# Kernel optimization log

Measured on AMD Instinct MI355X. Metric: run time of the kernel, lower is better.

Reference implementation:

```python
import jax, jax.numpy as jnp
import numpy as np
import math

B, SEQ_IN, D_IN = 4, 1028, 64
D = 1024          # hidden_size
H = 16            # num_heads
HD = D // H       # head_dim
L = 4             # num_layers
D_OUT = 1
EPS = 1e-6


def setup_inputs() -> dict:
    key = jax.random.key(0)
    ks = iter(jax.random.split(key, 32))
    s = 0.02
    inp = {}
    inp['x'] = jax.random.normal(next(ks), (B, SEQ_IN, D_IN), jnp.float32)
    # conv frontend (torch Conv1d weight layout: [out_ch, in_ch, k])
    inp['conv1_w'] = jax.random.normal(next(ks), (D // 2, D_IN, 3), jnp.float32) * s
    inp['conv1_b'] = jnp.zeros((D // 2,), jnp.float32)
    inp['conv2_w'] = jax.random.normal(next(ks), (D, D // 2, 3), jnp.float32) * s
    inp['conv2_b'] = jnp.zeros((D,), jnp.float32)
    # stacked per-layer params [L, ...]
    inp['lnA_w'] = jnp.ones((L, D), jnp.float32)
    inp['lnA_b'] = jnp.zeros((L, D), jnp.float32)
    inp['q_w'] = jax.random.normal(next(ks), (L, D, D), jnp.float32) * s
    inp['q_b'] = jnp.zeros((L, D), jnp.float32)
    inp['k_w'] = jax.random.normal(next(ks), (L, D, D), jnp.float32) * s
    inp['k_b'] = jnp.zeros((L, D), jnp.float32)
    inp['v_w'] = jax.random.normal(next(ks), (L, D, D), jnp.float32) * s
    inp['v_b'] = jnp.zeros((L, D), jnp.float32)
    inp['o_w'] = jax.random.normal(next(ks), (L, D, D), jnp.float32) * s
    inp['o_b'] = jnp.zeros((L, D), jnp.float32)
    inp['lnB_w'] = jnp.ones((L, D), jnp.float32)
    inp['lnB_b'] = jnp.zeros((L, D), jnp.float32)
    inp['f1_w'] = jax.random.normal(next(ks), (L, 2 * D, D), jnp.float32) * s
    inp['f1_b'] = jnp.zeros((L, 2 * D), jnp.float32)
    inp['f2_w'] = jax.random.normal(next(ks), (L, D, 2 * D), jnp.float32) * s
    inp['f2_b'] = jnp.zeros((L, D), jnp.float32)
    inp['fc_w'] = jax.random.normal(next(ks), (D_OUT, D), jnp.float32) * s
    inp['fc_b'] = jnp.zeros((D_OUT,), jnp.float32)
    return inp


def _layernorm(x, w, b):
    # torch-style: unbiased std (ddof=1), eps added to std (not var)
    mean = jnp.mean(x, axis=-1, keepdims=True)
    var = jnp.sum((x - mean) ** 2, axis=-1, keepdims=True) / (x.shape[-1] - 1)
    return w * ((x - mean) / (jnp.sqrt(var) + EPS)) + b


def _pos_encoding(S, d):
    pos = jnp.arange(S, dtype=jnp.float32)[:, None]
    div = jnp.exp(jnp.arange(0, d, 2, dtype=jnp.float32) * (-math.log(10000.0) / d))
    pe = jnp.zeros((S, d), jnp.float32)
    pe = pe.at[:, 0::2].set(jnp.sin(pos * div))
    pe = pe.at[:, 1::2].set(jnp.cos(pos * div))
    return pe


def _forward(x, conv1_w, conv1_b, conv2_w, conv2_b,
             lnA_w, lnA_b, q_w, q_b, k_w, k_b, v_w, v_b, o_w, o_b,
             lnB_w, lnB_b, f1_w, f1_b, f2_w, f2_b, fc_w, fc_b):
    dn = ('NCH', 'OIH', 'NCH')
    h = jnp.transpose(x, (0, 2, 1))                       # [B, D_in, S_in]
    h = jax.lax.conv_general_dilated(h, conv1_w, (1,), 'VALID', dimension_numbers=dn) + conv1_b[None, :, None]
    h = jax.lax.conv_general_dilated(h, conv2_w, (1,), 'VALID', dimension_numbers=dn) + conv2_b[None, :, None]
    h = jnp.transpose(h, (0, 2, 1))                       # [B, S, D]
    S = h.shape[1]
    h = h + _pos_encoding(S, D)[None]
    scale = 1.0 / math.sqrt(HD)

    def layer(xc, p):
        (lnaw, lnab, qw, qb, kw, kb, vw, vb, ow, ob,
         lnbw, lnbb, f1w, f1b, f2w, f2b) = p
        hn = _layernorm(xc, lnaw, lnab)
        q = (hn @ qw.T + qb).reshape(B, S, H, HD).transpose(0, 2, 1, 3)
        k = (hn @ kw.T + kb).reshape(B, S, H, HD).transpose(0, 2, 1, 3)
        v = (hn @ vw.T + vb).reshape(B, S, H, HD).transpose(0, 2, 1, 3)
        scores = jnp.einsum('bhsd,bhtd->bhst', q, k) * scale
        attn = scores / (1.0 + jnp.abs(scores))           # softsign, NOT softmax
        wv = jnp.einsum('bhst,bhtd->bhsd', attn, v)
        wv = wv.transpose(0, 2, 1, 3).reshape(B, S, D)
        xc = xc + (wv @ ow.T + ob)
        hn2 = _layernorm(xc, lnbw, lnbb)
        ff = jax.nn.relu(hn2 @ f1w.T + f1b) @ f2w.T + f2b
        return xc + ff, None

    params = (lnA_w, lnA_b, q_w, q_b, k_w, k_b, v_w, v_b, o_w, o_b,
              lnB_w, lnB_b, f1_w, f1_b, f2_w, f2_b)
    h, _ = jax.lax.scan(layer, h, params)
    pooled = jnp.mean(h, axis=1)                          # [B, D]
    return pooled @ fc_w.T + fc_b                         # [B, D_OUT]


def reference(x, conv1_w, conv1_b, conv2_w, conv2_b,
              lnA_w, lnA_b, q_w, q_b, k_w, k_b, v_w, v_b, o_w, o_b,
              lnB_w, lnB_b, f1_w, f1_b, f2_w, f2_b, fc_w, fc_b):
    return _forward(x, conv1_w, conv1_b, conv2_w, conv2_b,
                    lnA_w, lnA_b, q_w, q_b, k_w, k_b, v_w, v_b, o_w, o_b,
                    lnB_w, lnB_b, f1_w, f1_b, f2_w, f2_b, fc_w, fc_b)
```

## Files before the change

### kernel.cpp

```cpp
#include <hip/hip_runtime.h>
#include <hip/hip_bf16.h>
#include <math.h>

typedef __bf16 v8bf __attribute__((ext_vector_type(8)));
typedef float  v4f  __attribute__((ext_vector_type(4)));
typedef unsigned short v8us __attribute__((ext_vector_type(8)));

__device__ __forceinline__ unsigned short f2bfu(float f) {
    unsigned u = __builtin_bit_cast(unsigned, f);
    unsigned r = (u + 0x7fffu + ((u >> 16) & 1u)) >> 16;
    return (unsigned short)r;
}
__device__ __forceinline__ float bf2f(unsigned short u) {
    unsigned x = ((unsigned)u) << 16;
    return __builtin_bit_cast(float, x);
}

__device__ __forceinline__ long long swidx(int r, int k, int kt ) {
    return ((long long)((r >> 4) * kt + (k >> 5)) << 9)
         + (((k >> 3) & 3) << 7) + ((r & 15) << 3) + (k & 7);
}

#define GLDS16(g, s)                                                        \
    __builtin_amdgcn_global_load_lds(                                       \
        (const __attribute__((address_space(1))) void*)(g),                 \
        (__attribute__((address_space(3))) void*)(s), 16, 0, 0)

__global__ __launch_bounds__(256) void gemm_sw_k(
    const unsigned short* __restrict__ Asw,
    const unsigned short* __restrict__ Bsw,
    const float* __restrict__ bias,
    const float* __restrict__ res,
    float* __restrict__ Cf,
    unsigned short* __restrict__ Cb,
    unsigned short* __restrict__ Csw,
    unsigned short* __restrict__ Ct, int ctcol0,
    int M, int N, int K, int ldC, int relu)
{
    __shared__ __align__(16) unsigned short As[2][8][512];
    __shared__ __align__(16) unsigned short Bs[2][8][512];
    const int t = threadIdx.x;
    const int w = t >> 6;
    const int l = t & 63;

    int bx = blockIdx.x, by = blockIdx.y;
    {
        int nbx = gridDim.x;
        int nb  = nbx * gridDim.y;
        if ((nb & 7) == 0) {
            int bid = by * nbx + bx;
            int nid = (bid & 7) * (nb >> 3) + (bid >> 3);
            by = nid / nbx;
            bx = nid - by * nbx;
        }
    }
    const int m0 = by * 128;
    const int n0 = bx * 128;
    const int r16 = l & 15;
    const int qb  = l >> 4;
    const int wm = w >> 1, wn = w & 1;
    const int kt = K >> 5;

    const unsigned short* gA0 = Asw + (((long long)((m0 >> 4) + 2 * w) * kt) << 9) + l * 8;
    const unsigned short* gA1 = gA0 + ((long long)kt << 9);
    const unsigned short* gB0 = Bsw + (((long long)((n0 >> 4) + 2 * w) * kt) << 9) + l * 8;
    const unsigned short* gB1 = gB0 + ((long long)kt << 9);

    v4f acc[4][4];
#pragma unroll
    for (int i = 0; i < 4; i++)
#pragma unroll
        for (int j = 0; j < 4; j++) acc[i][j] = (v4f){0.f, 0.f, 0.f, 0.f};

    GLDS16(gA0, &As[0][2 * w + 0][0]);
    GLDS16(gA1, &As[0][2 * w + 1][0]);
    GLDS16(gB0, &Bs[0][2 * w + 0][0]);
    GLDS16(gB1, &Bs[0][2 * w + 1][0]);
    __syncthreads();

    int cur = 0;
    for (int c = 1; c < kt; c++) {
        const long long o = (long long)c << 9;
        GLDS16(gA0 + o, &As[cur ^ 1][2 * w + 0][0]);
        GLDS16(gA1 + o, &As[cur ^ 1][2 * w + 1][0]);
        GLDS16(gB0 + o, &Bs[cur ^ 1][2 * w + 0][0]);
        GLDS16(gB1 + o, &Bs[cur ^ 1][2 * w + 1][0]);
        v8bf af[4], bfr[4];
#pragma unroll
        for (int i = 0; i < 4; i++) af[i]  = *(const v8bf*)(&As[cur][4 * wm + i][l * 8]);
#pragma unroll
        for (int j = 0; j < 4; j++) bfr[j] = *(const v8bf*)(&Bs[cur][4 * wn + j][l * 8]);
#pragma unroll
        for (int i = 0; i < 4; i++)
#pragma unroll
            for (int j = 0; j < 4; j++)
                acc[i][j] = __builtin_amdgcn_mfma_f32_16x16x32_bf16(
                    af[i], bfr[j], acc[i][j], 0, 0, 0);
        __syncthreads();
        cur ^= 1;
    }
    {
        v8bf af[4], bfr[4];
#pragma unroll
        for (int i = 0; i < 4; i++) af[i]  = *(const v8bf*)(&As[cur][4 * wm + i][l * 8]);
#pragma unroll
        for (int j = 0; j < 4; j++) bfr[j] = *(const v8bf*)(&Bs[cur][4 * wn + j][l * 8]);
#pragma unroll
        for (int i = 0; i < 4; i++)
#pragma unroll
            for (int j = 0; j < 4; j++)
                acc[i][j] = __builtin_amdgcn_mfma_f32_16x16x32_bf16(
                    af[i], bfr[j], acc[i][j], 0, 0, 0);
    }

    float bv[4];
#pragma unroll
    for (int j = 0; j < 4; j++) bv[j] = bias[n0 + 64 * wn + 16 * j + r16];
    const int colbase = n0 + 64 * wn + r16;
    const int nt = N >> 5;
#pragma unroll
    for (int i = 0; i < 4; i++) {
        int rowb = m0 + 64 * wm + 16 * i + qb * 4;
#pragma unroll
        for (int j = 0; j < 4; j++) {
            int col = colbase + 16 * j;
            float v[4];
#pragma unroll
            for (int r = 0; r < 4; r++) v[r] = acc[i][j][r] + bv[j];
            if (Ct && col >= ctcol0) {
                ushort4 o;
                o.x = f2bfu(v[0]); o.y = f2bfu(v[1]);
                o.z = f2bfu(v[2]); o.w = f2bfu(v[3]);
                *(ushort4*)(Ct + ((long long)(rowb >> 10) << 20)
                            + (long long)(col - ctcol0) * 1024 + (rowb & 1023)) = o;
            } else if (Csw) {
#pragma unroll
                for (int r = 0; r < 4; r++) {
                    int row = rowb + r;
                    float vv = v[r];
                    if (relu) vv = fmaxf(vv, 0.f);
                    Csw[swidx(row, col, nt)] = f2bfu(vv);
                }
            } else {
#pragma unroll
                for (int r = 0; r < 4; r++) {
                    int row = rowb + r;
                    long long off = (long long)row * ldC + col;
                    float vv = v[r];
                    if (res)  vv += res[off];
                    if (relu) vv = fmaxf(vv, 0.f);
                    if (Cf) Cf[off] = vv;
                    if (Cb) ((unsigned short*)Cb)[off] = f2bfu(vv);
                }
            }
        }
    }
}

__global__ __launch_bounds__(256) void gemm_mfma_k(
    const __hip_bfloat16* __restrict__ A, int rpbA, long long bstrideA, int ldA,
    const __hip_bfloat16* __restrict__ B,
    const float* __restrict__ bias,
    const float* __restrict__ res,
    float* __restrict__ Cf,
    __hip_bfloat16* __restrict__ Cb,
    int M, int N, int K, int ldC, int relu)
{
    __shared__ __align__(16) __hip_bfloat16 As[2][8][64][8];
    __shared__ __align__(16) __hip_bfloat16 Bs[2][4][64][8];
    const int t  = threadIdx.x;
    const int w  = t >> 6;
    const int l  = t & 63;
    const int m0 = blockIdx.y * 128;
    const int n0 = blockIdx.x * 64;
    const int r16 = l & 15;
    const int qb  = l >> 4;
    const int wm = w >> 1, wn = w & 1;

    const __hip_bfloat16* gA[2];
#pragma unroll
    for (int tt = 0; tt < 2; tt++) {
        int arow = m0 + 16 * (2 * w + tt) + r16;
        gA[tt] = A + (long long)(arow / rpbA) * bstrideA
                   + (long long)(arow % rpbA) * ldA + qb * 8;
    }
    const __hip_bfloat16* gB = B + (long long)(n0 + 16 * w + r16) * K + qb * 8;

    v4f acc[4][2];
#pragma unroll
    for (int i = 0; i < 4; i++)
#pragma unroll
        for (int j = 0; j < 2; j++) acc[i][j] = (v4f){0.f, 0.f, 0.f, 0.f};

    GLDS16(gA[0], &As[0][2 * w + 0][0][0]);
    GLDS16(gA[1], &As[0][2 * w + 1][0][0]);
    GLDS16(gB,    &Bs[0][w][0][0]);
    __syncthreads();

    int cur = 0;
    for (int k0 = 32; k0 < K; k0 += 32) {
        v8bf af[4], bfr[2];
#pragma unroll
        for (int i = 0; i < 4; i++) af[i]  = *(const v8bf*)(&As[cur][4 * wm + i][l][0]);
#pragma unroll
        for (int j = 0; j < 2; j++) bfr[j] = *(const v8bf*)(&Bs[cur][2 * wn + j][l][0]);
        GLDS16(gA[0] + k0, &As[cur ^ 1][2 * w + 0][0][0]);
        GLDS16(gA[1] + k0, &As[cur ^ 1][2 * w + 1][0][0]);
        GLDS16(gB + k0,    &Bs[cur ^ 1][w][0][0]);
#pragma unroll
        for (int i = 0; i < 4; i++)
#pragma unroll
            for (int j = 0; j < 2; j++)
                acc[i][j] = __builtin_amdgcn_mfma_f32_16x16x32_bf16(
                    af[i], bfr[j], acc[i][j], 0, 0, 0);
        __syncthreads();
        cur ^= 1;
    }
    {
        v8bf af[4], bfr[2];
#pragma unroll
        for (int i = 0; i < 4; i++) af[i]  = *(const v8bf*)(&As[cur][4 * wm + i][l][0]);
#pragma unroll
        for (int j = 0; j < 2; j++) bfr[j] = *(const v8bf*)(&Bs[cur][2 * wn + j][l][0]);
#pragma unroll
        for (int i = 0; i < 4; i++)
#pragma unroll
            for (int j = 0; j < 2; j++)
                acc[i][j] = __builtin_amdgcn_mfma_f32_16x16x32_bf16(
                    af[i], bfr[j], acc[i][j], 0, 0, 0);
    }

    float bv[2];
#pragma unroll
    for (int j = 0; j < 2; j++) bv[j] = bias[n0 + 32 * wn + 16 * j + r16];
    const int colbase = n0 + 32 * wn + r16;
#pragma unroll
    for (int i = 0; i < 4; i++) {
        int rowb = m0 + 64 * wm + 16 * i + qb * 4;
#pragma unroll
        for (int j = 0; j < 2; j++) {
            int col = colbase + 16 * j;
#pragma unroll
            for (int r = 0; r < 4; r++) {
                int row = rowb + r;
                if (row >= M) continue;
                long long off = (long long)row * ldC + col;
                float vv = acc[i][j][r] + bv[j];
                if (res)  vv += res[off];
                if (relu) vv = fmaxf(vv, 0.f);
                if (Cf) Cf[off] = vv;
                if (Cb) ((unsigned short*)Cb)[off] = f2bfu(vv);
            }
        }
    }
}

__global__ __launch_bounds__(256) void attn_mfma_k(
    const unsigned short* __restrict__ QKV,
    const unsigned short* __restrict__ Vt,
    unsigned short* __restrict__ Osw)
{
    __shared__ __align__(16) unsigned short lds[25600];
    const int t = threadIdx.x, w = t >> 6, l = t & 63;
    const int bh = blockIdx.y, b = bh >> 4, h = bh & 15;
    const int s0 = blockIdx.x << 7;
    const int r16 = l & 15, q4 = l >> 4;
    const long long qrow0 = (long long)(b << 10) + s0;
    const int hoff = h << 6;

#pragma unroll
    for (int mi = 0; mi < 2; mi++)
#pragma unroll
        for (int kk = 0; kk < 2; kk++) {
            const unsigned short* g = QKV + (qrow0 + 32 * w + 16 * mi + r16) * 3072
                                      + hoff + 32 * kk + q4 * 8;
            GLDS16(g, &lds[(w * 4 + mi * 2 + kk) * 512]);
        }
    __syncthreads();
    v8bf qf[2][2];
#pragma unroll
    for (int mi = 0; mi < 2; mi++)
#pragma unroll
        for (int kk = 0; kk < 2; kk++)
            qf[mi][kk] = *(const v8bf*)&lds[(w * 4 + mi * 2 + kk) * 512 + l * 8];

    v4f oacc[2][4];
#pragma unroll
    for (int i = 0; i < 2; i++)
#pragma unroll
        for (int j = 0; j < 4; j++) oacc[i][j] = (v4f){0.f, 0.f, 0.f, 0.f};

    for (int t0 = 0; t0 < 1024; t0 += 64) {
#pragma unroll
        for (int rr = 0; rr < 2; rr++) {
            int r = 2 * w + rr, kk = r >> 2, j = r & 3;
            const unsigned short* gk = QKV
                + ((long long)(b << 10) + t0 + 16 * j + r16) * 3072
                + 1024 + hoff + 32 * kk + q4 * 8;
            GLDS16(gk, &lds[8192 + r * 512]);
            const unsigned short* gv = Vt + ((long long)b << 20)
                + (long long)(hoff + 16 * j + r16) * 1024 + t0 + 32 * kk + q4 * 8;
            GLDS16(gv, &lds[12288 + r * 512]);
        }
        __syncthreads();

        v8bf kf[2][4];
#pragma unroll
        for (int kk = 0; kk < 2; kk++)
#pragma unroll
            for (int j = 0; j < 4; j++)
                kf[kk][j] = *(const v8bf*)&lds[8192 + (kk * 4 + j) * 512 + l * 8];
        v4f sc[2][4];
#pragma unroll
        for (int i = 0; i < 2; i++)
#pragma unroll
            for (int j = 0; j < 4; j++) sc[i][j] = (v4f){0.f, 0.f, 0.f, 0.f};
#pragma unroll
        for (int kk = 0; kk < 2; kk++)
#pragma unroll
            for (int mi = 0; mi < 2; mi++)
#pragma unroll
                for (int j = 0; j < 4; j++)
                    sc[mi][j] = __builtin_amdgcn_mfma_f32_16x16x32_bf16(
                        qf[mi][kk], kf[kk][j], sc[mi][j], 0, 0, 0);

#pragma unroll
        for (int mi = 0; mi < 2; mi++)
#pragma unroll
            for (int j = 0; j < 4; j++)
#pragma unroll
                for (int r = 0; r < 4; r++) {
                    float v = sc[mi][j][r] * 0.125f;
                    float p = v * __builtin_amdgcn_rcpf(1.0f + fabsf(v));
                    lds[16384 + (32 * w + 16 * mi + q4 * 4 + r) * 72 + 16 * j + r16] = f2bfu(p);
                }

        v8bf pf[2][2], vf[2][4];
#pragma unroll
        for (int mi = 0; mi < 2; mi++)
#pragma unroll
            for (int kk = 0; kk < 2; kk++)
                pf[mi][kk] = *(const v8bf*)&lds[16384 + (32 * w + 16 * mi + r16) * 72
                                                + 32 * kk + q4 * 8];
#pragma unroll
        for (int kk = 0; kk < 2; kk++)
#pragma unroll
            for (int j = 0; j < 4; j++)
                vf[kk][j] = *(const v8bf*)&lds[12288 + (kk * 4 + j) * 512 + l * 8];
#pragma unroll
        for (int kk = 0; kk < 2; kk++)
#pragma unroll
            for (int mi = 0; mi < 2; mi++)
#pragma unroll
                for (int j = 0; j < 4; j++)
                    oacc[mi][j] = __builtin_amdgcn_mfma_f32_16x16x32_bf16(
                        pf[mi][kk], vf[kk][j], oacc[mi][j], 0, 0, 0);
        __syncthreads();
    }

#pragma unroll
    for (int mi = 0; mi < 2; mi++)
#pragma unroll
        for (int j = 0; j < 4; j++)
#pragma unroll
            for (int r = 0; r < 4; r++)
                lds[(32 * w + 16 * mi + q4 * 4 + r) * 72 + 16 * j + r16] =
                    f2bfu(oacc[mi][j][r]);
    __syncthreads();
    {
        int row = t >> 1, ch = (t & 1) << 5;
        int grow = (int)qrow0 + row;
#pragma unroll
        for (int i = 0; i < 4; i++) {
            int c0 = hoff + ch + 8 * i;
            v8us vv = *(const v8us*)&lds[row * 72 + ch + 8 * i];
            *(v8us*)(Osw + swidx(grow, c0, 32)) = vv;
        }
    }
}

__global__ __launch_bounds__(256) void layernorm_k(
    const float* __restrict__ x, const float* __restrict__ w,
    const float* __restrict__ b, unsigned short* __restrict__ ysw)
{
    int row = blockIdx.x;
    int t = threadIdx.x;
    float4 v = ((const float4*)(x + ((long long)row << 10)))[t];
    float s = v.x + v.y + v.z + v.w;
#pragma unroll
    for (int o = 32; o; o >>= 1) s += __shfl_down(s, o);
    __shared__ float red[4];
    __shared__ float red2[4];
    int wid = t >> 6, lane = t & 63;
    if (lane == 0) red[wid] = s;
    __syncthreads();
    float mean = (red[0] + red[1] + red[2] + red[3]) * (1.0f / 1024.0f);
    float dx = v.x - mean, dy = v.y - mean, dz = v.z - mean, dw = v.w - mean;
    float sq = dx * dx + dy * dy + dz * dz + dw * dw;
#pragma unroll
    for (int o = 32; o; o >>= 1) sq += __shfl_down(sq, o);
    if (lane == 0) red2[wid] = sq;
    __syncthreads();
    float var = (red2[0] + red2[1] + red2[2] + red2[3]) * (1.0f / 1023.0f);
    float inv = 1.0f / (sqrtf(var) + 1e-6f);
    float4 W  = ((const float4*)w)[t];
    float4 Bv = ((const float4*)b)[t];
    ushort4 o;
    o.x = f2bfu(W.x * (dx * inv) + Bv.x);
    o.y = f2bfu(W.y * (dy * inv) + Bv.y);
    o.z = f2bfu(W.z * (dz * inv) + Bv.z);
    o.w = f2bfu(W.w * (dw * inv) + Bv.w);
    int c0 = t << 2;
    *(ushort4*)(ysw + swidx(row, c0, 32)) = o;
}

__global__ __launch_bounds__(256) void add_pos_k(float* __restrict__ h)
{
    int idx = blockIdx.x * 256 + threadIdx.x;
    int d = idx & 1023;
    int s = (idx >> 10) & 1023;
    int e = d & ~1;
    float div = expf(-9.210340371976184f * (float)e * (1.0f / 1024.0f));
    float arg = (float)s * div;
    float pe = (d & 1) ? cosf(arg) : sinf(arg);
    h[idx] += pe;
}

__global__ __launch_bounds__(256) void convert_k(
    const float* __restrict__ src, unsigned short* __restrict__ dst, int n4)
{
    int i = blockIdx.x * 256 + threadIdx.x;
    if (i >= n4) return;
    float4 v = ((const float4*)src)[i];
    ushort4 o;
    o.x = f2bfu(v.x); o.y = f2bfu(v.y); o.z = f2bfu(v.z); o.w = f2bfu(v.w);
    ((ushort4*)dst)[i] = o;
}

__global__ __launch_bounds__(256) void convert_layer_sw_k(
    const float* __restrict__ q, const float* __restrict__ k,
    const float* __restrict__ v, const float* __restrict__ o,
    const float* __restrict__ f1, const float* __restrict__ f2,
    unsigned short* __restrict__ dst)
{
    int idx = blockIdx.x * 256 + threadIdx.x;
    const float* src;
    unsigned short* db;
    int Ksh, rf;
    if (idx < 0x100000) {
        int region = idx >> 18;
        rf = idx & 0x3FFFF;
        src = (region == 0) ? q : (region == 1) ? k : (region == 2) ? v : o;
        db = dst + ((long long)region << 20);
        Ksh = 10;
    } else if (idx < 0x180000) {
        rf = idx - 0x100000; src = f1; db = dst + (4LL << 20); Ksh = 10;
    } else {
        rf = idx - 0x180000; src = f2; db = dst + (6LL << 20); Ksh = 11;
    }
    float4 vv = ((const float4*)src)[rf];
    int flatf = rf << 2;
    int n  = flatf >> Ksh;
    int k0 = flatf & ((1 << Ksh) - 1);
    ushort4 ov;
    ov.x = f2bfu(vv.x); ov.y = f2bfu(vv.y); ov.z = f2bfu(vv.z); ov.w = f2bfu(vv.w);
    *(ushort4*)(db + swidx(n, k0, 1 << (Ksh - 5))) = ov;
}

__global__ __launch_bounds__(256) void concat3_k(
    const float* __restrict__ a, const float* __restrict__ b,
    const float* __restrict__ c, float* __restrict__ o)
{
    int i = blockIdx.x * 256 + threadIdx.x;
    o[i] = (i < 1024) ? a[i] : ((i < 2048) ? b[i - 1024] : c[i - 2048]);
}

__global__ __launch_bounds__(256) void reorder_w_k(
    const float* __restrict__ src, unsigned short* __restrict__ dst, int OC, int IC)
{
    int idx = blockIdx.x * 256 + threadIdx.x;
    if (idx >= OC * IC * 3) return;
    int k  = idx % 3;
    int ic = (idx / 3) % IC;
    int oc = idx / (3 * IC);
    dst[(oc * 3 + k) * IC + ic] = f2bfu(src[idx]);
}

__global__ __launch_bounds__(256) void meanpool_part_k(
    const float* __restrict__ h, float* __restrict__ part)
{
    int g = blockIdx.x;
    int b = g >> 6, rblk = g & 63;
    const float4* base = (const float4*)(h + ((long long)b << 20)
                                           + ((long long)(rblk * 16) << 10));
    float4 s = {0.f, 0.f, 0.f, 0.f};
#pragma unroll
    for (int i = 0; i < 16; i++) {
        float4 v = base[i * 256 + threadIdx.x];
        s.x += v.x; s.y += v.y; s.z += v.z; s.w += v.w;
    }
    ((float4*)part)[g * 256 + threadIdx.x] = s;
}

__global__ __launch_bounds__(256) void meanpool_red_k(
    const float* __restrict__ part, float* __restrict__ pooled)
{
    int idx = blockIdx.x * 256 + threadIdx.x;
    int b = idx >> 10, d = idx & 1023;
    const float* p = part + ((long long)(b * 64) << 10) + d;
    float s = 0.f;
#pragma unroll 8
    for (int r = 0; r < 64; r++) s += p[r << 10];
    pooled[idx] = s * (1.0f / 1024.0f);
}

__global__ __launch_bounds__(256) void fc_k(
    const float* __restrict__ p, const float* __restrict__ w,
    const float* __restrict__ fb, float* __restrict__ out)
{
    int b = blockIdx.x, t = threadIdx.x;
    float s = 0.f;
    for (int i = t; i < 1024; i += 256) s += p[(b << 10) + i] * w[i];
#pragma unroll
    for (int o = 32; o; o >>= 1) s += __shfl_down(s, o);
    __shared__ float red[4];
    if ((t & 63) == 0) red[t >> 6] = s;
    __syncthreads();
    if (t == 0) out[b] = red[0] + red[1] + red[2] + red[3] + fb[0];
}

extern "C" void kernel_launch(void* const* d_in, const int* in_sizes, int n_in,
                              void* d_out, int out_size, void* d_ws, size_t ws_size,
                              hipStream_t stream)
{
    const float* x    = (const float*)d_in[0];
    const float* c1w  = (const float*)d_in[1];
    const float* c1b  = (const float*)d_in[2];
    const float* c2w  = (const float*)d_in[3];
    const float* c2b  = (const float*)d_in[4];
    const float* lnAw = (const float*)d_in[5];
    const float* lnAb = (const float*)d_in[6];
    const float* qw   = (const float*)d_in[7];
    const float* qbi  = (const float*)d_in[8];
    const float* kw   = (const float*)d_in[9];
    const float* kbi  = (const float*)d_in[10];
    const float* vw   = (const float*)d_in[11];
    const float* vbi  = (const float*)d_in[12];
    const float* ow   = (const float*)d_in[13];
    const float* obi  = (const float*)d_in[14];
    const float* lnBw = (const float*)d_in[15];
    const float* lnBb = (const float*)d_in[16];
    const float* f1w  = (const float*)d_in[17];
    const float* f1b  = (const float*)d_in[18];
    const float* f2w  = (const float*)d_in[19];
    const float* f2b  = (const float*)d_in[20];
    const float* fcw  = (const float*)d_in[21];
    const float* fcb  = (const float*)d_in[22];
    float* out = (float*)d_out;

    float* ws = (float*)d_ws;
    typedef __hip_bfloat16 bf;
    typedef unsigned short us;
    float* h    = ws;
    us* hn_b    = (us*)(ws + 4194304);
    us* qkv_b   = (us*)(ws + 6291456);
    us* ff_b    = qkv_b;
    us* wq_b    = (us*)(ws + 12582912);
    us* wo_b    = (us*)(ws + 14155776);
    us* wf1_b   = (us*)(ws + 14680064);
    us* wf2_b   = (us*)(ws + 15728640);
    us* xb      = (us*)(ws + 16777216);
    us* h1b     = (us*)(ws + 16912896);
    us* w1t_b   = (us*)(ws + 17963520);
    us* w2t_b   = (us*)(ws + 18012672);
    float* pooled = ws + 18799104;
    us* Vt      = (us*)(ws + 18803200);
    float* bqkv = ws + 20900352;
    float* mp_part = ws + 20903424;

    convert_k<<<dim3(257), 256, 0, stream>>>(x, xb, 65792);
    reorder_w_k<<<dim3(384),  256, 0, stream>>>(c1w, w1t_b, 512, 64);
    reorder_w_k<<<dim3(6144), 256, 0, stream>>>(c2w, w2t_b, 1024, 512);

    gemm_mfma_k<<<dim3(8, 33), 256, 0, stream>>>(
        (const bf*)xb, 1026, 1028LL * 64, 64, (const bf*)w1t_b,
        c1b, nullptr, nullptr, (bf*)h1b, 4104, 512, 192, 512, 0);
    gemm_mfma_k<<<dim3(16, 32), 256, 0, stream>>>(
        (const bf*)h1b, 1024, 1026LL * 512, 512, (const bf*)w2t_b,
        c2b, nullptr, h, nullptr, 4096, 1024, 1536, 1024, 0);
    add_pos_k<<<dim3(16384), 256, 0, stream>>>(h);

    for (int l = 0; l < 4; l++) {
        long long wo  = (long long)l * 1048576;
        long long wo2 = (long long)l * 2097152;
        convert_layer_sw_k<<<dim3(8192), 256, 0, stream>>>(
            qw + wo, kw + wo, vw + wo, ow + wo, f1w + wo2, f2w + wo2, wq_b);
        concat3_k<<<dim3(12), 256, 0, stream>>>(qbi + l * 1024, kbi + l * 1024,
                                                vbi + l * 1024, bqkv);

        layernorm_k<<<dim3(4096), 256, 0, stream>>>(h, lnAw + l * 1024, lnAb + l * 1024, hn_b);
        gemm_sw_k<<<dim3(24, 32), 256, 0, stream>>>(
            hn_b, wq_b, bqkv, nullptr, nullptr, qkv_b, nullptr, Vt, 2048,
            4096, 3072, 1024, 3072, 0);
        attn_mfma_k<<<dim3(8, 64), 256, 0, stream>>>(qkv_b, Vt, hn_b);
        gemm_sw_k<<<dim3(8, 32), 256, 0, stream>>>(
            hn_b, wo_b, obi + l * 1024, h, h, nullptr, nullptr, nullptr, 0,
            4096, 1024, 1024, 1024, 0);
        layernorm_k<<<dim3(4096), 256, 0, stream>>>(h, lnBw + l * 1024, lnBb + l * 1024, hn_b);
        gemm_sw_k<<<dim3(16, 32), 256, 0, stream>>>(
            hn_b, wf1_b, f1b + l * 2048, nullptr, nullptr, nullptr, ff_b, nullptr, 0,
            4096, 2048, 1024, 2048, 1);
        gemm_sw_k<<<dim3(8, 32), 256, 0, stream>>>(
            ff_b, wf2_b, f2b + l * 1024, h, h, nullptr, nullptr, nullptr, 0,
            4096, 1024, 2048, 1024, 0);
    }

    meanpool_part_k<<<dim3(256), 256, 0, stream>>>(h, mp_part);
    meanpool_red_k<<<dim3(16), 256, 0, stream>>>(mp_part, pooled);
    fc_k<<<dim3(4), 256, 0, stream>>>(pooled, fcw, fcb, out);
}
```

Measured before the change: 1.279 ms.

## Load GEMM operand fragments directly from global into registers, dropping LDS staging

```diff
diff --git a/kernel.cpp b/kernel.cpp
--- a/kernel.cpp
+++ b/kernel.cpp
@@ -37,8 +37,6 @@
     unsigned short* __restrict__ Ct, int ctcol0,
     int M, int N, int K, int ldC, int relu)
 {
-    __shared__ __align__(16) unsigned short As[2][8][512];
-    __shared__ __align__(16) unsigned short Bs[2][8][512];
     const int t = threadIdx.x;
     const int w = t >> 6;
     const int l = t & 63;
@@ -61,10 +59,14 @@
     const int wm = w >> 1, wn = w & 1;
     const int kt = K >> 5;
 
-    const unsigned short* gA0 = Asw + (((long long)((m0 >> 4) + 2 * w) * kt) << 9) + l * 8;
-    const unsigned short* gA1 = gA0 + ((long long)kt << 9);
-    const unsigned short* gB0 = Bsw + (((long long)((n0 >> 4) + 2 * w) * kt) << 9) + l * 8;
-    const unsigned short* gB1 = gB0 + ((long long)kt << 9);
+    const unsigned short* pa[4];
+#pragma unroll
+    for (int i = 0; i < 4; i++)
+        pa[i] = Asw + ((long long)(((m0 >> 4) + 4 * wm + i) * kt) << 9) + l * 8;
+    const unsigned short* pb[4];
+#pragma unroll
+    for (int j = 0; j < 4; j++)
+        pb[j] = Bsw + ((long long)(((n0 >> 4) + 4 * wn + j) * kt) << 9) + l * 8;
 
     v4f acc[4][4];
 #pragma unroll
@@ -72,45 +74,39 @@
 #pragma unroll
         for (int j = 0; j < 4; j++) acc[i][j] = (v4f){0.f, 0.f, 0.f, 0.f};
 
-    GLDS16(gA0, &As[0][2 * w + 0][0]);
-    GLDS16(gA1, &As[0][2 * w + 1][0]);
-    GLDS16(gB0, &Bs[0][2 * w + 0][0]);
-    GLDS16(gB1, &Bs[0][2 * w + 1][0]);
-    __syncthreads();
-
-    int cur = 0;
-    for (int c = 1; c < kt; c++) {
-        const long long o = (long long)c << 9;
-        GLDS16(gA0 + o, &As[cur ^ 1][2 * w + 0][0]);
-        GLDS16(gA1 + o, &As[cur ^ 1][2 * w + 1][0]);
-        GLDS16(gB0 + o, &Bs[cur ^ 1][2 * w + 0][0]);
-        GLDS16(gB1 + o, &Bs[cur ^ 1][2 * w + 1][0]);
-        v8bf af[4], bfr[4];
-#pragma unroll
-        for (int i = 0; i < 4; i++) af[i]  = *(const v8bf*)(&As[cur][4 * wm + i][l * 8]);
-#pragma unroll
-        for (int j = 0; j < 4; j++) bfr[j] = *(const v8bf*)(&Bs[cur][4 * wn + j][l * 8]);
+    v8bf A0[4], A1[4], B0[4], B1[4];
+#pragma unroll
+    for (int i = 0; i < 4; i++) A0[i] = *(const v8bf*)(pa[i]);
+#pragma unroll
+    for (int j = 0; j < 4; j++) B0[j] = *(const v8bf*)(pb[j]);
+
+    for (int s = 0; s < kt; s += 2) {
+        {
+            const long long o = (long long)(s + 1) << 9;
+#pragma unroll
+            for (int i = 0; i < 4; i++) A1[i] = *(const v8bf*)(pa[i] + o);
+#pragma unroll
+            for (int j = 0; j < 4; j++) B1[j] = *(const v8bf*)(pb[j] + o);
+        }
 #pragma unroll
         for (int i = 0; i < 4; i++)
 #pragma unroll
             for (int j = 0; j < 4; j++)
                 acc[i][j] = __builtin_amdgcn_mfma_f32_16x16x32_bf16(
-                    af[i], bfr[j], acc[i][j], 0, 0, 0);
-        __syncthreads();
-        cur ^= 1;
-    }
-    {
-        v8bf af[4], bfr[4];
-#pragma unroll
-        for (int i = 0; i < 4; i++) af[i]  = *(const v8bf*)(&As[cur][4 * wm + i][l * 8]);
-#pragma unroll
-        for (int j = 0; j < 4; j++) bfr[j] = *(const v8bf*)(&Bs[cur][4 * wn + j][l * 8]);
+                    A0[i], B0[j], acc[i][j], 0, 0, 0);
+        if (s + 2 < kt) {
+            const long long o = (long long)(s + 2) << 9;
+#pragma unroll
+            for (int i = 0; i < 4; i++) A0[i] = *(const v8bf*)(pa[i] + o);
+#pragma unroll
+            for (int j = 0; j < 4; j++) B0[j] = *(const v8bf*)(pb[j] + o);
+        }
 #pragma unroll
         for (int i = 0; i < 4; i++)
 #pragma unroll
             for (int j = 0; j < 4; j++)
                 acc[i][j] = __builtin_amdgcn_mfma_f32_16x16x32_bf16(
-                    af[i], bfr[j], acc[i][j], 0, 0, 0);
+                    A1[i], B1[j], acc[i][j], 0, 0, 0);
     }
 
     float bv[4];
```

Measured after the change: 1.164 ms. -9.0%, faster.

## Deepen GEMM LDS pipeline to four stages with explicit vmcnt waits

Applied to the files above, without the earlier changes.

```diff
diff --git a/kernel.cpp b/kernel.cpp
--- a/kernel.cpp
+++ b/kernel.cpp
@@ -25,6 +25,12 @@
     __builtin_amdgcn_global_load_lds(                                       \
         (const __attribute__((address_space(1))) void*)(g),                 \
         (__attribute__((address_space(3))) void*)(s), 16, 0, 0)
+
+#define BARRIER() asm volatile("s_barrier" ::: "memory")
+#define WAITC(n) do {                                                       \
+    asm volatile("s_waitcnt vmcnt(" #n ")" ::: "memory");                   \
+    __builtin_amdgcn_sched_barrier(0);                                      \
+} while (0)
 
 __global__ __launch_bounds__(256) void gemm_sw_k(
     const unsigned short* __restrict__ Asw,
@@ -37,8 +43,8 @@
     unsigned short* __restrict__ Ct, int ctcol0,
     int M, int N, int K, int ldC, int relu)
 {
-    __shared__ __align__(16) unsigned short As[2][8][512];
-    __shared__ __align__(16) unsigned short Bs[2][8][512];
+    __shared__ __align__(16) unsigned short As[4][8][512];
+    __shared__ __align__(16) unsigned short Bs[4][8][512];
     const int t = threadIdx.x;
     const int w = t >> 6;
     const int l = t & 63;
@@ -72,46 +78,48 @@
 #pragma unroll
         for (int j = 0; j < 4; j++) acc[i][j] = (v4f){0.f, 0.f, 0.f, 0.f};
 
-    GLDS16(gA0, &As[0][2 * w + 0][0]);
-    GLDS16(gA1, &As[0][2 * w + 1][0]);
-    GLDS16(gB0, &Bs[0][2 * w + 0][0]);
-    GLDS16(gB1, &Bs[0][2 * w + 1][0]);
-    __syncthreads();
-
-    int cur = 0;
-    for (int c = 1; c < kt; c++) {
-        const long long o = (long long)c << 9;
-        GLDS16(gA0 + o, &As[cur ^ 1][2 * w + 0][0]);
-        GLDS16(gA1 + o, &As[cur ^ 1][2 * w + 1][0]);
-        GLDS16(gB0 + o, &Bs[cur ^ 1][2 * w + 0][0]);
-        GLDS16(gB1 + o, &Bs[cur ^ 1][2 * w + 1][0]);
-        v8bf af[4], bfr[4];
-#pragma unroll
-        for (int i = 0; i < 4; i++) af[i]  = *(const v8bf*)(&As[cur][4 * wm + i][l * 8]);
-#pragma unroll
-        for (int j = 0; j < 4; j++) bfr[j] = *(const v8bf*)(&Bs[cur][4 * wn + j][l * 8]);
-#pragma unroll
-        for (int i = 0; i < 4; i++)
-#pragma unroll
-            for (int j = 0; j < 4; j++)
-                acc[i][j] = __builtin_amdgcn_mfma_f32_16x16x32_bf16(
-                    af[i], bfr[j], acc[i][j], 0, 0, 0);
-        __syncthreads();
-        cur ^= 1;
-    }
-    {
-        v8bf af[4], bfr[4];
-#pragma unroll
-        for (int i = 0; i < 4; i++) af[i]  = *(const v8bf*)(&As[cur][4 * wm + i][l * 8]);
-#pragma unroll
-        for (int j = 0; j < 4; j++) bfr[j] = *(const v8bf*)(&Bs[cur][4 * wn + j][l * 8]);
-#pragma unroll
-        for (int i = 0; i < 4; i++)
-#pragma unroll
-            for (int j = 0; j < 4; j++)
-                acc[i][j] = __builtin_amdgcn_mfma_f32_16x16x32_bf16(
-                    af[i], bfr[j], acc[i][j], 0, 0, 0);
-    }
+#define STAGE(c) do {                                                       \
+    const int b_ = (c) & 3;                                                 \
+    const long long o_ = (long long)(c) << 9;                               \
+    GLDS16(gA0 + o_, &As[b_][2 * w + 0][0]);                                \
+    GLDS16(gA1 + o_, &As[b_][2 * w + 1][0]);                                \
+    GLDS16(gB0 + o_, &Bs[b_][2 * w + 0][0]);                                \
+    GLDS16(gB1 + o_, &Bs[b_][2 * w + 1][0]);                                \
+} while (0)
+
+#define COMPUTE(c) do {                                                     \
+    const int b_ = (c) & 3;                                                 \
+    v8bf af_[4], bf_[4];                                                    \
+    _Pragma("unroll")                                                       \
+    for (int i_ = 0; i_ < 4; i_++)                                          \
+        af_[i_] = *(const v8bf*)(&As[b_][4 * wm + i_][l * 8]);              \
+    _Pragma("unroll")                                                       \
+    for (int j_ = 0; j_ < 4; j_++)                                          \
+        bf_[j_] = *(const v8bf*)(&Bs[b_][4 * wn + j_][l * 8]);              \
+    _Pragma("unroll")                                                       \
+    for (int i_ = 0; i_ < 4; i_++)                                          \
+    _Pragma("unroll")                                                       \
+    for (int j_ = 0; j_ < 4; j_++)                                          \
+        acc[i_][j_] = __builtin_amdgcn_mfma_f32_16x16x32_bf16(              \
+            af_[i_], bf_[j_], acc[i_][j_], 0, 0, 0);                        \
+} while (0)
+
+    STAGE(0); STAGE(1); STAGE(2);
+
+    int c = 0;
+    for (; c < kt - 3; ++c) {
+        STAGE(c + 3);
+        WAITC(12);
+        BARRIER();
+        COMPUTE(c);
+        BARRIER();
+    }
+    WAITC(8);  BARRIER(); COMPUTE(kt - 3); BARRIER();
+    WAITC(4);  BARRIER(); COMPUTE(kt - 2); BARRIER();
+    WAITC(0);  BARRIER(); COMPUTE(kt - 1);
+
+#undef STAGE
+#undef COMPUTE
 
     float bv[4];
 #pragma unroll
```

New measurement: 1.269 ms. About the same (-0.8%).
